# Kernel optimization log

Measured on AMD Instinct MI355X. Metric: run time of the kernel, lower is better.

The kernel has to match this reference:

```python
import jax, jax.numpy as jnp
import numpy as np
from jax import lax

T, B, D, H = 512, 2048, 64, 10  # time, batch, input_dim, hidden_dim (= n_qubits)
CLIP = 5.0


def setup_inputs() -> dict:
    key = jax.random.key(0)
    ks = jax.random.split(key, 5)
    inputs = jax.random.normal(ks[0], (T, B, D), jnp.float32)

    def lin(k):
        kw, kb = jax.random.split(k)
        W = jax.random.normal(kw, (H, D + H), jnp.float32) * 0.1
        b = jax.random.normal(kb, (H,), jnp.float32) * 0.1
        return W, b

    Wf, bf = lin(ks[1])
    Wi, bi = lin(ks[2])
    Wu, bu = lin(ks[3])
    Wo, bo = lin(ks[4])
    return dict(inputs=inputs, Wf=Wf, bf=bf, Wi=Wi, bi=bi,
                Wu=Wu, bu=bu, Wo=Wo, bo=bo)


def _quantum_gate(p):
    # Analytic statevector result: RX(p_q) per qubit then CX chain q->q+1.
    # <Z_q> = prod_{j<=q} cos(p_j); Qiskit big-endian labels reverse the order.
    return jnp.flip(jnp.cumprod(jnp.cos(p), axis=-1), axis=-1)


def _fcl(hx):
    # RY(hx_q) per qubit, measure Z on qubit n-1 (label 'Z'+'I'*(n-1)) -> cos(hx[:, -1])
    return jnp.cos(hx[:, -1:])  # [B, 1]


def reference(inputs, Wf, bf, Wi, bi, Wu, bu, Wo, bo):
    Bsz = inputs.shape[1]
    Hd = Wf.shape[0]
    h0 = jnp.zeros((Bsz, Hd), inputs.dtype)
    c0 = jnp.zeros((Bsz, Hd), inputs.dtype)

    def step(carry, x):
        hx, cx = carry
        comb = jnp.concatenate([x, hx], axis=1)  # [B, D+H]
        clip = lambda z: jnp.clip(z, -CLIP, CLIP)
        f = jax.nn.sigmoid(_quantum_gate(clip(comb @ Wf.T + bf)))
        i = jax.nn.sigmoid(_quantum_gate(clip(comb @ Wi.T + bi)))
        g = jnp.tanh(_quantum_gate(clip(comb @ Wu.T + bu)))
        o = jax.nn.sigmoid(_quantum_gate(clip(comb @ Wo.T + bo)))
        cx = f * cx + i * g
        hx = o * jnp.tanh(cx)
        hx = hx * _fcl(hx)  # scalar modulation broadcast over hidden dim
        return (hx, cx), hx

    (hx, cx), outputs = lax.scan(step, (h0, c0), inputs)
    return outputs, (hx, cx)
```

## Files before the change

kernel.cpp:

```cpp
#include <hip/hip_runtime.h>

#define TT   512
#define BATCH 2048
#define DIN  64
#define HD   10

__global__ __launch_bounds__(64, 2)
void qlstm_kernel(const float* __restrict__ X,
                  const float* __restrict__ Wf, const float* __restrict__ bf,
                  const float* __restrict__ Wi, const float* __restrict__ bi,
                  const float* __restrict__ Wu, const float* __restrict__ bu,
                  const float* __restrict__ Wo, const float* __restrict__ bo,
                  float* __restrict__ out)
{
    const int row  = blockIdx.x;
    const int lane = threadIdx.x;
    const int g    = lane / HD;
    const int q    = lane - g * HD;
    const int gb   = g * HD;

    __shared__ float xs[2][DIN];

    const float LOG2E = 1.4426950408889634f;
    const float INV2PI = 0.15915494309189535f;

    float wx[DIN];
    float wh[HD];
    float bias = 0.f;
    float cmul = -LOG2E, amul = 1.f, aadd = 0.f;

    const float* Wg = Wf; const float* bg = bf;
    if (g == 1) { Wg = Wi; bg = bi; }
    else if (g == 2) { Wg = Wu; bg = bu; cmul = -2.f * LOG2E; amul = 2.f; aadd = -1.f; }
    else if (g == 3) { Wg = Wo; bg = bo; }

    if (lane < 4 * HD) {
        #pragma unroll
        for (int k = 0; k < DIN; ++k) wx[k] = Wg[q * (DIN + HD) + k];
        #pragma unroll
        for (int k = 0; k < HD; ++k)  wh[k] = Wg[q * (DIN + HD) + DIN + k];
        bias = bg[q];
    } else {
        #pragma unroll
        for (int k = 0; k < DIN; ++k) wx[k] = 0.f;
        #pragma unroll
        for (int k = 0; k < HD; ++k)  wh[k] = 0.f;
    }

    float h[HD];
    #pragma unroll
    for (int k = 0; k < HD; ++k) h[k] = 0.f;
    float c = 0.f;
    float hlast = 0.f;

    const size_t xstep = (size_t)BATCH * DIN;

    xs[0][lane] = X[(size_t)row * DIN + lane];

    int cur = 0;
    for (int t = 0; t < TT; ++t) {
        float xn = 0.f;
        if (t + 1 < TT) xn = X[(size_t)(t + 1) * xstep + (size_t)row * DIN + lane];

        float z = bias;
        #pragma unroll
        for (int k4 = 0; k4 < DIN / 4; ++k4) {
            float4 xq = *reinterpret_cast<const float4*>(&xs[cur][k4 * 4]);
            z += wx[k4 * 4 + 0] * xq.x;
            z += wx[k4 * 4 + 1] * xq.y;
            z += wx[k4 * 4 + 2] * xq.z;
            z += wx[k4 * 4 + 3] * xq.w;
        }
        #pragma unroll
        for (int k = 0; k < HD; ++k) z += wh[k] * h[k];

        z = fminf(fmaxf(z, -5.f), 5.f);
        float p = __builtin_amdgcn_cosf(z * INV2PI);

        #pragma unroll
        for (int off = 1; off < 16; off <<= 1) {
            float other = __shfl(p, lane - off);
            p = (q >= off) ? p * other : p;
        }
        float G = __shfl(p, gb + (HD - 1) - q);

        float e = __builtin_amdgcn_exp2f(cmul * G);
        float r = __builtin_amdgcn_rcpf(1.f + e);
        float a = amul * r + aadd;

        float fg = __shfl(a, q);
        float ig = __shfl(a, HD + q);
        float ug = __shfl(a, 2 * HD + q);
        float og = __shfl(a, 3 * HD + q);

        c = fg * c + ig * ug;
        float e2 = __builtin_amdgcn_exp2f(-2.f * LOG2E * c);
        float th = 2.f * __builtin_amdgcn_rcpf(1.f + e2) - 1.f;
        float hpre = og * th;
        float h9 = __int_as_float(__builtin_amdgcn_readlane(__float_as_int(hpre), 9));
        float m = __builtin_amdgcn_cosf(h9 * INV2PI);
        float hnew = hpre * m;
        hlast = hnew;

        #pragma unroll
        for (int k = 0; k < HD; ++k)
            h[k] = __int_as_float(__builtin_amdgcn_readlane(__float_as_int(hnew), k));

        if (lane < HD) out[((size_t)t * BATCH + row) * HD + lane] = hnew;

        int nxt = cur ^ 1;
        if (t + 1 < TT) xs[nxt][lane] = xn;
        cur = nxt;
    }

    if (lane < HD) {
        size_t base = (size_t)TT * BATCH * HD;
        out[base + (size_t)row * HD + lane] = hlast;
        out[base + (size_t)BATCH * HD + (size_t)row * HD + lane] = c;
    }
}

extern "C" void kernel_launch(void* const* d_in, const int* in_sizes, int n_in,
                              void* d_out, int out_size, void* d_ws, size_t ws_size,
                              hipStream_t stream) {
    const float* X  = (const float*)d_in[0];
    const float* Wf = (const float*)d_in[1];
    const float* bf = (const float*)d_in[2];
    const float* Wi = (const float*)d_in[3];
    const float* bi = (const float*)d_in[4];
    const float* Wu = (const float*)d_in[5];
    const float* bu = (const float*)d_in[6];
    const float* Wo = (const float*)d_in[7];
    const float* bo = (const float*)d_in[8];
    float* out = (float*)d_out;

    qlstm_kernel<<<BATCH, 64, 0, stream>>>(X, Wf, bf, Wi, bi, Wu, bu, Wo, bo, out);
}
```

Measured before the change: 757.0 us.

## Remap gates to 16-lane rows, use DPP prefix scan, precompute input projection

Measured after the change: 638.5 us. -15.7%, faster.

```diff
diff --git a/kernel.cpp b/kernel.cpp
--- a/kernel.cpp
+++ b/kernel.cpp
@@ -1,9 +1,10 @@
 #include <hip/hip_runtime.h>
 
-#define TT   512
+#define TT    512
 #define BATCH 2048
-#define DIN  64
-#define HD   10
+#define DIN   64
+#define HD    10
+#define WROW  (DIN + HD)
 
 __global__ __launch_bounds__(64, 2)
 void qlstm_kernel(const float* __restrict__ X,
@@ -15,31 +16,31 @@
 {
     const int row  = blockIdx.x;
     const int lane = threadIdx.x;
-    const int g    = lane / HD;
-    const int q    = lane - g * HD;
-    const int gb   = g * HD;
+    const int g    = lane >> 4;
+    const int v    = lane & 15;
+    const bool act_lane = (v >= 6);
 
     __shared__ float xs[2][DIN];
 
-    const float LOG2E = 1.4426950408889634f;
+    const float LOG2E  = 1.4426950408889634f;
     const float INV2PI = 0.15915494309189535f;
 
-    float wx[DIN];
-    float wh[HD];
-    float bias = 0.f;
     float cmul = -LOG2E, amul = 1.f, aadd = 0.f;
-
     const float* Wg = Wf; const float* bg = bf;
     if (g == 1) { Wg = Wi; bg = bi; }
     else if (g == 2) { Wg = Wu; bg = bu; cmul = -2.f * LOG2E; amul = 2.f; aadd = -1.f; }
     else if (g == 3) { Wg = Wo; bg = bo; }
 
-    if (lane < 4 * HD) {
+    float wx[DIN];
+    float wh[HD];
+    float bias = 0.f;
+    if (act_lane) {
+        const int uw = 15 - v;
         #pragma unroll
-        for (int k = 0; k < DIN; ++k) wx[k] = Wg[q * (DIN + HD) + k];
+        for (int k = 0; k < DIN; ++k) wx[k] = Wg[uw * WROW + k];
         #pragma unroll
-        for (int k = 0; k < HD; ++k)  wh[k] = Wg[q * (DIN + HD) + DIN + k];
-        bias = bg[q];
+        for (int k = 0; k < HD; ++k)  wh[k] = Wg[uw * WROW + DIN + k];
+        bias = bg[uw];
     } else {
         #pragma unroll
         for (int k = 0; k < DIN; ++k) wx[k] = 0.f;
@@ -51,72 +52,99 @@
     #pragma unroll
     for (int k = 0; k < HD; ++k) h[k] = 0.f;
     float c = 0.f;
-    float hlast = 0.f;
+    float hkeep = 0.f;
 
     const size_t xstep = (size_t)BATCH * DIN;
+    const size_t xbase = (size_t)row * DIN + lane;
 
-    xs[0][lane] = X[(size_t)row * DIN + lane];
+    xs[0][lane] = X[xbase];
+    float xr = X[xstep + xbase];
+
+    float zx;
+    {
+        float s0 = bias, s1 = 0.f, s2 = 0.f, s3 = 0.f;
+        #pragma unroll
+        for (int k = 0; k < DIN; k += 4) {
+            float4 xq = *reinterpret_cast<const float4*>(&xs[0][k]);
+            s0 = fmaf(wx[k + 0], xq.x, s0);
+            s1 = fmaf(wx[k + 1], xq.y, s1);
+            s2 = fmaf(wx[k + 2], xq.z, s2);
+            s3 = fmaf(wx[k + 3], xq.w, s3);
+        }
+        zx = (s0 + s1) + (s2 + s3);
+    }
 
     int cur = 0;
     for (int t = 0; t < TT; ++t) {
-        float xn = 0.f;
-        if (t + 1 < TT) xn = X[(size_t)(t + 1) * xstep + (size_t)row * DIN + lane];
+        const int nxt = cur ^ 1;
+        if (t + 1 < TT) xs[nxt][lane] = xr;
+        if (t + 2 < TT) xr = X[(size_t)(t + 2) * xstep + xbase];
 
-        float z = bias;
+        float za = zx, zb = 0.f;
         #pragma unroll
-        for (int k4 = 0; k4 < DIN / 4; ++k4) {
-            float4 xq = *reinterpret_cast<const float4*>(&xs[cur][k4 * 4]);
-            z += wx[k4 * 4 + 0] * xq.x;
-            z += wx[k4 * 4 + 1] * xq.y;
-            z += wx[k4 * 4 + 2] * xq.z;
-            z += wx[k4 * 4 + 3] * xq.w;
+        for (int j = 0; j < HD; j += 2) {
+            za = fmaf(wh[j],     h[j],     za);
+            zb = fmaf(wh[j + 1], h[j + 1], zb);
         }
-        #pragma unroll
-        for (int k = 0; k < HD; ++k) z += wh[k] * h[k];
-
+        float z = za + zb;
         z = fminf(fmaxf(z, -5.f), 5.f);
         float p = __builtin_amdgcn_cosf(z * INV2PI);
 
-        #pragma unroll
-        for (int off = 1; off < 16; off <<= 1) {
-            float other = __shfl(p, lane - off);
-            p = (q >= off) ? p * other : p;
+        {
+            int s_;
+            s_ = __builtin_amdgcn_update_dpp(0x3f800000, __float_as_int(p), 0x101, 0xF, 0xF, false);
+            p *= __int_as_float(s_);
+            s_ = __builtin_amdgcn_update_dpp(0x3f800000, __float_as_int(p), 0x102, 0xF, 0xF, false);
+            p *= __int_as_float(s_);
+            s_ = __builtin_amdgcn_update_dpp(0x3f800000, __float_as_int(p), 0x104, 0xF, 0xF, false);
+            p *= __int_as_float(s_);
+            s_ = __builtin_amdgcn_update_dpp(0x3f800000, __float_as_int(p), 0x108, 0xF, 0xF, false);
+            p *= __int_as_float(s_);
         }
-        float G = __shfl(p, gb + (HD - 1) - q);
 
-        float e = __builtin_amdgcn_exp2f(cmul * G);
-        float r = __builtin_amdgcn_rcpf(1.f + e);
-        float a = amul * r + aadd;
+        float e = __builtin_amdgcn_exp2f(cmul * p);
+        float a = amul * __builtin_amdgcn_rcpf(1.f + e) + aadd;
 
-        float fg = __shfl(a, q);
-        float ig = __shfl(a, HD + q);
-        float ug = __shfl(a, 2 * HD + q);
-        float og = __shfl(a, 3 * HD + q);
+        float fg = __shfl(a, v);
+        float ig = __shfl(a, 16 + v);
+        float ug = __shfl(a, 32 + v);
+        float og = __shfl(a, 48 + v);
 
-        c = fg * c + ig * ug;
+        c = fmaf(fg, c, ig * ug);
         float e2 = __builtin_amdgcn_exp2f(-2.f * LOG2E * c);
         float th = 2.f * __builtin_amdgcn_rcpf(1.f + e2) - 1.f;
         float hpre = og * th;
-        float h9 = __int_as_float(__builtin_amdgcn_readlane(__float_as_int(hpre), 9));
-        float m = __builtin_amdgcn_cosf(h9 * INV2PI);
+        float h9 = __int_as_float(__builtin_amdgcn_readlane(__float_as_int(hpre), 15));
+        float m  = __builtin_amdgcn_cosf(h9 * INV2PI);
         float hnew = hpre * m;
-        hlast = hnew;
+        hkeep = hnew;
+
+        if (lane >= 6 && lane < 16) out[((size_t)t * BATCH + row) * HD + (lane - 6)] = hnew;
 
         #pragma unroll
-        for (int k = 0; k < HD; ++k)
-            h[k] = __int_as_float(__builtin_amdgcn_readlane(__float_as_int(hnew), k));
+        for (int j = 0; j < HD; ++j)
+            h[j] = __int_as_float(__builtin_amdgcn_readlane(__float_as_int(hnew), 6 + j));
 
-        if (lane < HD) out[((size_t)t * BATCH + row) * HD + lane] = hnew;
-
-        int nxt = cur ^ 1;
-        if (t + 1 < TT) xs[nxt][lane] = xn;
+        if (t + 1 < TT) {
+            float s0 = bias, s1 = 0.f, s2 = 0.f, s3 = 0.f;
+            const float* xp = xs[nxt];
+            #pragma unroll
+            for (int k = 0; k < DIN; k += 4) {
+                float4 xq = *reinterpret_cast<const float4*>(&xp[k]);
+                s0 = fmaf(wx[k + 0], xq.x, s0);
+                s1 = fmaf(wx[k + 1], xq.y, s1);
+                s2 = fmaf(wx[k + 2], xq.z, s2);
+                s3 = fmaf(wx[k + 3], xq.w, s3);
+            }
+            zx = (s0 + s1) + (s2 + s3);
+        }
         cur = nxt;
     }
 
-    if (lane < HD) {
-        size_t base = (size_t)TT * BATCH * HD;
-        out[base + (size_t)row * HD + lane] = hlast;
-        out[base + (size_t)BATCH * HD + (size_t)row * HD + lane] = c;
+    if (lane >= 6 && lane < 16) {
+        const size_t base = (size_t)TT * BATCH * HD;
+        out[base + (size_t)row * HD + (lane - 6)] = hkeep;
+        out[base + (size_t)BATCH * HD + (size_t)row * HD + (lane - 6)] = c;
     }
 }
 
```
